# Kernel optimization log

Hardware: AMD Instinct MI355X
Metric: run time of the kernel (lower is better)

## Reference

```python
import jax, jax.numpy as jnp
import numpy as np

D_MODEL = 2048
NUM_HEADS = 32
HEAD_DIM = D_MODEL // NUM_HEADS  # 64
ROPE_BASE = 10000.0


def _rope_cos_sin(seq_len, head_dim, dtype):
    inv_freq = 1.0 / (ROPE_BASE ** (jnp.arange(0, head_dim, 2, dtype=jnp.float32) / head_dim))
    freqs = jnp.arange(seq_len, dtype=jnp.float32)[:, None] * inv_freq[None, :]  # (S, Dh/2)
    emb = jnp.concatenate([freqs, freqs], axis=-1)  # (S, Dh)
    return emb.astype(dtype), jnp.cos(emb).astype(dtype), jnp.sin(emb).astype(dtype)


def _rotate_half(x):
    x1, x2 = jnp.split(x, 2, axis=-1)
    return jnp.concatenate([-x2, x1], axis=-1)


def setup_inputs() -> dict:
    key = jax.random.key(0)
    k1, k2, k3, k4 = jax.random.split(key, 4)
    B, S, D = 1, 2048, D_MODEL
    x = jax.random.normal(k1, (B, S, D), dtype=jnp.float32)
    Wqkv = jax.random.normal(k2, (3 * D, D), dtype=jnp.float32) * 0.02
    Wo = jax.random.normal(k3, (D, D), dtype=jnp.float32) * 0.02
    gate = jax.random.normal(k4, (D,), dtype=jnp.float32) * 0.1
    return {"x": x, "Wqkv": Wqkv, "Wo": Wo, "gate": gate}


def reference(x, Wqkv, Wo, gate):
    B, S, D = x.shape
    H, Dh = NUM_HEADS, HEAD_DIM
    residual = x

    # fused QKV projection (torch Linear: y = x @ W.T)
    qkv = jnp.einsum('bsd,ed->bse', x, Wqkv).reshape(B, S, 3, H, Dh)
    q, k, v = qkv[:, :, 0], qkv[:, :, 1], qkv[:, :, 2]  # each (B, S, H, Dh)

    # RoPE
    _, cos, sin = _rope_cos_sin(S, Dh, x.dtype)
    cos = cos[None, :, None, :]  # (1, S, 1, Dh)
    sin = sin[None, :, None, :]
    q = q * cos + _rotate_half(q) * sin
    k = k * cos + _rotate_half(k) * sin

    # causal SDPA
    scale = 1.0 / np.sqrt(Dh)
    scores = jnp.einsum('bqhd,bkhd->bhqk', q, k) * scale  # (B, H, S, S)
    causal = jnp.tril(jnp.ones((S, S), dtype=bool))
    scores = jnp.where(causal[None, None], scores, jnp.finfo(scores.dtype).min)
    probs = jax.nn.softmax(scores, axis=-1)
    attn = jnp.einsum('bhqk,bkhd->bqhd', probs, v).reshape(B, S, D)

    out = jnp.einsum('bsd,ed->bse', attn, Wo)
    # HeoGate: learned per-channel gated residual (assumption; see notes)
    return residual + gate * out
```

## Files before the change

### kernel.cpp

```cpp
#include <hip/hip_runtime.h>
#include <hip/hip_bf16.h>
#include <cstdint>
#include <cstddef>

typedef __hip_bfloat16 bf16;
typedef short short8 __attribute__((ext_vector_type(8)));
typedef float f32x4 __attribute__((ext_vector_type(4)));

#define S_LEN 2048
#define DMODEL 2048
#define NQKV 6144
#define NHEADS 32
#define HDIM 64
#define ROPE_L2 0.4152410118609203f

__device__ __forceinline__ void async_copy16(const bf16* g, bf16* l) {
  __builtin_amdgcn_global_load_lds(
      (const __attribute__((address_space(1))) void*)g,
      (__attribute__((address_space(3))) void*)l, 16, 0, 0);
}

__device__ __forceinline__ f32x4 mfma_bf16(short8 a, short8 b, f32x4 c) {
  return __builtin_amdgcn_mfma_f32_16x16x32_bf16(a, b, c, 0, 0, 0);
}

__global__ __launch_bounds__(256) void cvt3_kernel(const float* __restrict__ sx,
                                                   bf16* __restrict__ dx,
                                                   const float* __restrict__ sw,
                                                   bf16* __restrict__ dw,
                                                   const float* __restrict__ so,
                                                   bf16* __restrict__ dov) {
  int i = blockIdx.x * 256 + threadIdx.x;
  const float* s;
  bf16* d;
  if (i < 1048576) {
    s = sx; d = dx;
  } else if (i < 4194304) {
    s = sw; d = dw; i -= 1048576;
  } else {
    s = so; d = dov; i -= 4194304;
  }
  const float4 v = ((const float4*)s)[i];
  union { bf16 h[4]; ushort4 u; } tmp;
  tmp.h[0] = __float2bfloat16(v.x);
  tmp.h[1] = __float2bfloat16(v.y);
  tmp.h[2] = __float2bfloat16(v.z);
  tmp.h[3] = __float2bfloat16(v.w);
  ((ushort4*)d)[i] = tmp.u;
}

#define QKV_NT 32
#define QBAR() do { __builtin_amdgcn_s_barrier(); __builtin_amdgcn_sched_barrier(0); } while (0)
#define WAITV(n) asm volatile("s_waitcnt vmcnt(" #n ")" ::: "memory")
#define LGKM0() do { asm volatile("s_waitcnt lgkmcnt(0)" ::: "memory"); \
                     __builtin_amdgcn_sched_barrier(0); } while (0)

__global__ __launch_bounds__(512, 2) void gemm_qkv(const bf16* __restrict__ A,
                                                   const bf16* __restrict__ W,
                                                   bf16* __restrict__ q_ws,
                                                   bf16* __restrict__ k_ws,
                                                   bf16* __restrict__ v_ws) {
  __shared__ bf16 smem[65536];
  const int tid = threadIdx.x;
  const int wave = tid >> 6, lane = tid & 63;
  const int wm = wave >> 2, wn = wave & 3;
  const int m0 = blockIdx.y * 256, n0 = blockIdx.x * 256;
  const int swc = (((lane & 3) ^ ((lane >> 3) & 3)) * 8);
  const int fr = lane & 15, fq = lane >> 4;
  const int rdc = ((fq ^ ((fr >> 1) & 3)) * 8);
  const int srg = wave * 16 + (lane >> 2);

  auto stageA = [&](int t_, int kk_, int off_) {
#pragma unroll
    for (int rd = 0; rd < 2; ++rd)
      async_copy16(A + (size_t)(m0 + rd * 128 + srg) * DMODEL + t_ * 64 + kk_ * 32 + swc,
                   &smem[off_ + (rd * 128 + wave * 16) * 32]);
  };
  auto stageB = [&](int t_, int kk_, int off_) {
#pragma unroll
    for (int rd = 0; rd < 2; ++rd)
      async_copy16(W + (size_t)(n0 + rd * 128 + srg) * DMODEL + t_ * 64 + kk_ * 32 + swc,
                   &smem[off_ + (rd * 128 + wave * 16) * 32]);
  };

  const f32x4 zero = {0.f, 0.f, 0.f, 0.f};
  f32x4 acc[8][4];
#pragma unroll
  for (int i = 0; i < 8; ++i)
#pragma unroll
    for (int j = 0; j < 4; ++j) acc[i][j] = zero;
  short8 a[4], b[4];

  stageA(0, 0, 0);
  stageB(0, 0, 16384);
  stageA(0, 1, 8192);
  stageB(0, 1, 24576);
  stageA(1, 0, 32768);
  stageB(1, 0, 32768 + 16384);
  WAITV(8);
  QBAR();

#define LOAD_A(KK, MB, BC)                                                        \
  {                                                                               \
    const bf16* sA_ = &smem[(BC) * 32768 + (KK) * 8192];                          \
    _Pragma("unroll") for (int mi = 0; mi < 4; ++mi)                              \
        a[mi] = *(const short8*)&sA_[(wm * 128 + (MB) + mi * 16 + fr) * 32 + rdc];\
  }
#define LOAD_B(KK, BC)                                                            \
  {                                                                               \
    const bf16* sB_ = &smem[(BC) * 32768 + 16384 + (KK) * 8192];                  \
    _Pragma("unroll") for (int n = 0; n < 4; ++n)                                 \
        b[n] = *(const short8*)&sB_[(wn * 64 + n * 16 + fr) * 32 + rdc];          \
  }
#define MFMA16(MB)                                                                \
  __builtin_amdgcn_s_setprio(1);                                                  \
  _Pragma("unroll") for (int mi = 0; mi < 4; ++mi)                                \
      _Pragma("unroll") for (int n = 0; n < 4; ++n)                               \
          acc[(MB) / 16 + mi][n] = mfma_bf16(a[mi], b[n], acc[(MB) / 16 + mi][n]);\
  __builtin_amdgcn_s_setprio(0);

#pragma unroll 2
  for (int t = 0; t < QKV_NT; ++t) {
    const int bc = t & 1, bn = bc ^ 1;
    LOAD_A(0, 0, bc); LOAD_B(0, bc);
    if (t + 1 < QKV_NT) stageA(t + 1, 1, bn * 32768 + 8192);
    QBAR(); LGKM0();
    MFMA16(0);
    QBAR();
    LOAD_A(0, 64, bc);
    if (t + 1 < QKV_NT) stageB(t + 1, 1, bn * 32768 + 24576);
    QBAR(); LGKM0();
    MFMA16(64);
    if (t < QKV_NT - 1) { WAITV(8); } else { WAITV(0); }
    QBAR();
    LOAD_A(1, 64, bc); LOAD_B(1, bc);
    if (t + 2 < QKV_NT) stageA(t + 2, 0, bc * 32768);
    QBAR(); LGKM0();
    MFMA16(64);
    QBAR();
    LOAD_A(1, 0, bc);
    if (t + 2 < QKV_NT) stageB(t + 2, 0, bc * 32768 + 16384);
    QBAR(); LGKM0();
    MFMA16(0);
    if (t < QKV_NT - 2) { WAITV(8); }
    else if (t == QKV_NT - 2) { WAITV(4); }
    QBAR();
  }
#undef LOAD_A
#undef LOAD_B
#undef MFMA16

  const int colb = n0 + wn * 64;
  const int sect = colb >> 11;
  const int h = (colb & 2047) >> 6;
  const int col = fr, rq = fq * 4;

  if (sect < 2) {
    bf16* dst = ((sect == 0) ? q_ws : k_ws) + (size_t)h * S_LEN * HDIM;
    bf16* rep = smem + wave * 1152;
    const float f0 = exp2f(-(float)col * ROPE_L2);
    const float f1 = exp2f(-(float)(16 + col) * ROPE_L2);
    __syncthreads();
    for (int m = 0; m < 8; ++m) {
      const int base_s = m0 + wm * 128 + m * 16;
#pragma unroll
      for (int jl = 0; jl < 2; ++jl) {
        const int dh = jl * 16 + col;
        const float fr_ = (jl == 0) ? f0 : f1;
#pragma unroll
        for (int r = 0; r < 4; ++r) {
          const int srow = base_s + rq + r;
          float sn, cs;
          __sincosf((float)srow * fr_, &sn, &cs);
          const float xl = acc[m][jl][r], xh = acc[m][jl + 2][r];
          rep[(rq + r) * 72 + dh]      = __float2bfloat16(xl * cs - xh * sn);
          rep[(rq + r) * 72 + dh + 32] = __float2bfloat16(xh * cs + xl * sn);
        }
      }
#pragma unroll
      for (int p = 0; p < 2; ++p) {
        const int rr = p * 8 + (lane >> 3), ch = lane & 7;
        const uint4 vv = *(const uint4*)&rep[rr * 72 + ch * 8];
        *(uint4*)&dst[(size_t)(base_s + rr) * HDIM + ch * 8] = vv;
      }
    }
  } else {
    bf16* dst = v_ws + (size_t)h * HDIM * S_LEN;
    for (int j = 0; j < 4; ++j) {
      const int dh = j * 16 + col;
      for (int m = 0; m < 8; ++m) {
        const int s0 = m0 + wm * 128 + m * 16 + rq;
        union { bf16 hx[4]; uint2 u; } vk;
#pragma unroll
        for (int r = 0; r < 4; ++r) vk.hx[r] = __float2bfloat16(acc[m][j][r]);
        *(uint2*)&dst[(size_t)dh * S_LEN + s0] = vk.u;
      }
    }
  }
}

__global__ __launch_bounds__(256) void attn_kernel(const bf16* __restrict__ q_ws,
                                                   const bf16* __restrict__ k_ws,
                                                   const bf16* __restrict__ vt_ws,
                                                   bf16* __restrict__ attn_out) {
  const int bid = blockIdx.x;
  const int qt = 31 - (bid >> 5);
  const int h = bid & 31;

  const int tid = threadIdx.x, wave = tid >> 6, lane = tid & 63;
  const int col = lane & 15, fq = lane >> 4;
  const int q_glob = qt * 64 + wave * 16 + col;

  __shared__ bf16 Ks[2][64 * 64];
  __shared__ bf16 Vs[2][64 * 64];
  __shared__ bf16 Pl[4][16 * 72];
  bf16* pl = Pl[wave];

  const bf16* qh = q_ws + (size_t)h * S_LEN * HDIM;
  const bf16* kh = k_ws + (size_t)h * S_LEN * HDIM;
  const bf16* vh = vt_ws + (size_t)h * HDIM * S_LEN;

  const int srow = lane >> 3;
  const int slot = lane & 7;
  const int schunk = slot ^ srow;

  auto stage = [&](int kt, int buf) {
    const int k0 = kt * 64;
#pragma unroll
    for (int j = 0; j < 2; ++j) {
      const int r8 = (wave * 2 + j) * 8;
      async_copy16(kh + (size_t)(k0 + r8 + srow) * HDIM + schunk * 8,
                   &Ks[buf][r8 * 64]);
      async_copy16(vh + (size_t)(r8 + srow) * S_LEN + k0 + schunk * 8,
                   &Vs[buf][r8 * 64]);
    }
  };

  short8 qf[2];
#pragma unroll
  for (int ks = 0; ks < 2; ++ks)
    qf[ks] = *(const short8*)&qh[(size_t)q_glob * HDIM + ks * 32 + fq * 8];

  const f32x4 zero = {0.f, 0.f, 0.f, 0.f};
  f32x4 o_acc[4] = {zero, zero, zero, zero};
  float m_i = -1e30f, l_i = 0.f;

  stage(0, 0);

  for (int kt = 0; kt <= qt; ++kt) {
    const int buf = kt & 1;
    const int k0 = kt * 64;
    __syncthreads();
    if (kt < qt) stage(kt + 1, buf ^ 1);

    short8 kf[8];
#pragma unroll
    for (int n = 0; n < 4; ++n) {
      const int row = n * 16 + col;
#pragma unroll
      for (int ks = 0; ks < 2; ++ks)
        kf[n * 2 + ks] =
            *(const short8*)&Ks[buf][row * 64 + (((ks * 4 + fq) ^ (row & 7)) * 8)];
    }
    f32x4 s_acc[4] = {zero, zero, zero, zero};
#pragma unroll
    for (int n = 0; n < 4; ++n)
#pragma unroll
      for (int ks = 0; ks < 2; ++ks)
        s_acc[n] = mfma_bf16(kf[n * 2 + ks], qf[ks], s_acc[n]);

    short8 vf[8];
#pragma unroll
    for (int n = 0; n < 4; ++n) {
      const int row = n * 16 + col;
#pragma unroll
      for (int ks = 0; ks < 2; ++ks)
        vf[n * 2 + ks] =
            *(const short8*)&Vs[buf][row * 64 + (((ks * 4 + fq) ^ (row & 7)) * 8)];
    }

    if (kt == qt) {
#pragma unroll
      for (int n = 0; n < 4; ++n)
#pragma unroll
        for (int r = 0; r < 4; ++r)
          if (k0 + n * 16 + fq * 4 + r > q_glob) s_acc[n][r] = -1e30f;
    }

    float vmax = -1e30f;
#pragma unroll
    for (int n = 0; n < 4; ++n)
#pragma unroll
      for (int r = 0; r < 4; ++r) vmax = fmaxf(vmax, s_acc[n][r]);
    vmax = fmaxf(vmax, __shfl_xor(vmax, 16, 64));
    vmax = fmaxf(vmax, __shfl_xor(vmax, 32, 64));
    const float mnew = fmaxf(m_i, vmax);
    const float alpha = __expf((m_i - mnew) * 0.125f);
    m_i = mnew;

    float rs = 0.f;
#pragma unroll
    for (int n = 0; n < 4; ++n)
#pragma unroll
      for (int r = 0; r < 4; ++r) {
        const float p = __expf((s_acc[n][r] - mnew) * 0.125f);
        s_acc[n][r] = p;
        rs += p;
      }
    rs += __shfl_xor(rs, 16, 64);
    rs += __shfl_xor(rs, 32, 64);
    l_i = l_i * alpha + rs;

#pragma unroll
    for (int n = 0; n < 4; ++n)
#pragma unroll
      for (int r = 0; r < 4; ++r) o_acc[n][r] *= alpha;

#pragma unroll
    for (int n = 0; n < 4; ++n) {
      union { bf16 hx[4]; uint2 u; } pk;
#pragma unroll
      for (int r = 0; r < 4; ++r) pk.hx[r] = __float2bfloat16(s_acc[n][r]);
      *(uint2*)&pl[col * 72 + n * 16 + fq * 4] = pk.u;
    }
    short8 pa[2];
#pragma unroll
    for (int ks = 0; ks < 2; ++ks)
      pa[ks] = *(const short8*)&pl[col * 72 + ks * 32 + fq * 8];

#pragma unroll
    for (int n = 0; n < 4; ++n)
#pragma unroll
      for (int ks = 0; ks < 2; ++ks)
        o_acc[n] = mfma_bf16(vf[n * 2 + ks], pa[ks], o_acc[n]);
  }

  const float inv = 1.0f / l_i;
#pragma unroll
  for (int n = 0; n < 4; ++n) {
#pragma unroll
    for (int r = 0; r < 4; ++r) o_acc[n][r] *= inv;
    union { bf16 hx[4]; uint2 u; } ok;
#pragma unroll
    for (int r = 0; r < 4; ++r) ok.hx[r] = __float2bfloat16(o_acc[n][r]);
    *(uint2*)&attn_out[(size_t)q_glob * DMODEL + h * HDIM + n * 16 + fq * 4] = ok.u;
  }
}

__global__ __launch_bounds__(256) void gemm_out(const bf16* __restrict__ A,
                                                const bf16* __restrict__ W,
                                                const float* __restrict__ xres,
                                                const float* __restrict__ gate,
                                                float* __restrict__ out) {
  constexpr int K = DMODEL;
  __shared__ bf16 As[64 * 32];
  __shared__ bf16 Bs[128 * 32];
  const int tid = threadIdx.x;
  const int wave = tid >> 6, lane = tid & 63;
  const int m0 = blockIdx.y * 64, n0 = blockIdx.x * 128;
  const int sr = lane >> 2;
  const int swc = (((lane & 3) ^ ((lane >> 3) & 3)) * 8);
  const int fr = lane & 15, fq = lane >> 4;
  const int rdc = ((fq ^ ((fr >> 1) & 3)) * 8);

  const f32x4 zero = {0.f, 0.f, 0.f, 0.f};
  f32x4 acc[4][2];
  for (int i = 0; i < 4; ++i)
    for (int j = 0; j < 2; ++j) acc[i][j] = zero;

  for (int kt = 0; kt < K; kt += 32) {
    __syncthreads();
    async_copy16(A + (size_t)(m0 + wave * 16 + sr) * K + kt + swc,
                 &As[(wave * 16) * 32]);
#pragma unroll
    for (int j = 0; j < 2; ++j)
      async_copy16(W + (size_t)(n0 + wave * 32 + j * 16 + sr) * K + kt + swc,
                   &Bs[(wave * 32 + j * 16) * 32]);
    __syncthreads();
    short8 a[4], b[2];
    for (int i = 0; i < 4; ++i)
      a[i] = *(const short8*)&As[(i * 16 + fr) * 32 + rdc];
    for (int j = 0; j < 2; ++j)
      b[j] = *(const short8*)&Bs[(wave * 32 + j * 16 + fr) * 32 + rdc];
    for (int i = 0; i < 4; ++i)
      for (int j = 0; j < 2; ++j)
        acc[i][j] = mfma_bf16(a[i], b[j], acc[i][j]);
  }

  const int col = fr, rq = fq * 4;
  for (int j = 0; j < 2; ++j) {
    const int cc = n0 + wave * 32 + j * 16 + col;
    const float g = gate[cc];
    for (int i = 0; i < 4; ++i) {
      const int base_row = m0 + i * 16 + rq;
      for (int r = 0; r < 4; ++r) {
        const size_t idx = (size_t)(base_row + r) * DMODEL + cc;
        out[idx] = xres[idx] + g * acc[i][j][r];
      }
    }
  }
}

extern "C" void kernel_launch(void* const* d_in, const int* in_sizes, int n_in,
                              void* d_out, int out_size, void* d_ws, size_t ws_size,
                              hipStream_t stream) {
  const float* x    = (const float*)d_in[0];
  const float* Wqkv = (const float*)d_in[1];
  const float* Wo   = (const float*)d_in[2];
  const float* gate = (const float*)d_in[3];
  float* out = (float*)d_out;

  char* ws = (char*)d_ws;
  const size_t MB = 1024 * 1024;
  bf16* xb      = (bf16*)(ws);
  bf16* wqkvb   = (bf16*)(ws + 8 * MB);
  bf16* wob     = (bf16*)(ws + 32 * MB);
  bf16* q_ws    = (bf16*)(ws + 40 * MB);
  bf16* k_ws    = (bf16*)(ws + 48 * MB);
  bf16* v_ws    = (bf16*)(ws + 56 * MB);
  bf16* attn_ws = (bf16*)(ws);

  cvt3_kernel<<<dim3(20480), 256, 0, stream>>>(x, xb, Wqkv, wqkvb, Wo, wob);

  gemm_qkv<<<dim3(NQKV / 256, S_LEN / 256), 512, 0, stream>>>(xb, wqkvb, q_ws, k_ws, v_ws);
  attn_kernel<<<dim3(1024), 256, 0, stream>>>(q_ws, k_ws, v_ws, attn_ws);
  gemm_out<<<dim3(DMODEL / 128, DMODEL / 64), 256, 0, stream>>>(attn_ws, wob, x, gate, out);
}
```

Measured before the change: 253.1 us.

## Widen attention tiles, add lazy softmax rescaling, triple-buffer output GEMM

The attention kernel now processes 128 query rows per block with 8 waves, so each staged K/V tile is shared by twice as many queries. Online-softmax rescaling is skipped unless some lane's running max grows by more than a threshold, which drops exp and multiply work on most iterations. The output GEMM gains a 3-stage async LDS pipeline with vmcnt waits, overlapping loads with MFMA work. In exchange, the larger blocks halve the grid and lengthen per-block causal work, and the diff relies on WAITV/QBAR/LGKM0 macros that must already be defined in the unseen part of the file.

```diff
diff --git a/kernel.cpp b/kernel.cpp
--- a/kernel.cpp
+++ b/kernel.cpp
@@ -199,21 +199,21 @@
   }
 }
 
-__global__ __launch_bounds__(256) void attn_kernel(const bf16* __restrict__ q_ws,
+__global__ __launch_bounds__(512) void attn_kernel(const bf16* __restrict__ q_ws,
                                                    const bf16* __restrict__ k_ws,
                                                    const bf16* __restrict__ vt_ws,
                                                    bf16* __restrict__ attn_out) {
   const int bid = blockIdx.x;
-  const int qt = 31 - (bid >> 5);
+  const int qt = 15 - (bid >> 5);
   const int h = bid & 31;
 
   const int tid = threadIdx.x, wave = tid >> 6, lane = tid & 63;
   const int col = lane & 15, fq = lane >> 4;
-  const int q_glob = qt * 64 + wave * 16 + col;
+  const int q_glob = qt * 128 + wave * 16 + col;
 
   __shared__ bf16 Ks[2][64 * 64];
   __shared__ bf16 Vs[2][64 * 64];
-  __shared__ bf16 Pl[4][16 * 72];
+  __shared__ bf16 Pl[8][16 * 72];
   bf16* pl = Pl[wave];
 
   const bf16* qh = q_ws + (size_t)h * S_LEN * HDIM;
@@ -226,14 +226,11 @@
 
   auto stage = [&](int kt, int buf) {
     const int k0 = kt * 64;
-#pragma unroll
-    for (int j = 0; j < 2; ++j) {
-      const int r8 = (wave * 2 + j) * 8;
-      async_copy16(kh + (size_t)(k0 + r8 + srow) * HDIM + schunk * 8,
-                   &Ks[buf][r8 * 64]);
-      async_copy16(vh + (size_t)(r8 + srow) * S_LEN + k0 + schunk * 8,
-                   &Vs[buf][r8 * 64]);
-    }
+    const int r8 = wave * 8;
+    async_copy16(kh + (size_t)(k0 + r8 + srow) * HDIM + schunk * 8,
+                 &Ks[buf][r8 * 64]);
+    async_copy16(vh + (size_t)(r8 + srow) * S_LEN + k0 + schunk * 8,
+                 &Vs[buf][r8 * 64]);
   };
 
   short8 qf[2];
@@ -247,11 +244,12 @@
 
   stage(0, 0);
 
-  for (int kt = 0; kt <= qt; ++kt) {
+  const int lastk = 2 * qt + 1;
+  for (int kt = 0; kt <= lastk; ++kt) {
     const int buf = kt & 1;
     const int k0 = kt * 64;
     __syncthreads();
-    if (kt < qt) stage(kt + 1, buf ^ 1);
+    if (kt < lastk) stage(kt + 1, buf ^ 1);
 
     short8 kf[8];
 #pragma unroll
@@ -279,7 +277,7 @@
             *(const short8*)&Vs[buf][row * 64 + (((ks * 4 + fq) ^ (row & 7)) * 8)];
     }
 
-    if (kt == qt) {
+    if (k0 + 63 > qt * 128 + wave * 16) {
 #pragma unroll
       for (int n = 0; n < 4; ++n)
 #pragma unroll
@@ -294,27 +292,30 @@
       for (int r = 0; r < 4; ++r) vmax = fmaxf(vmax, s_acc[n][r]);
     vmax = fmaxf(vmax, __shfl_xor(vmax, 16, 64));
     vmax = fmaxf(vmax, __shfl_xor(vmax, 32, 64));
-    const float mnew = fmaxf(m_i, vmax);
-    const float alpha = __expf((m_i - mnew) * 0.125f);
-    m_i = mnew;
+
+    if (!__all(vmax - m_i <= 8.0f)) {
+      const float mnew = fmaxf(m_i, vmax);
+      const float alpha = __expf((m_i - mnew) * 0.125f);
+      l_i *= alpha;
+#pragma unroll
+      for (int n = 0; n < 4; ++n)
+#pragma unroll
+        for (int r = 0; r < 4; ++r) o_acc[n][r] *= alpha;
+      m_i = mnew;
+    }
 
     float rs = 0.f;
 #pragma unroll
     for (int n = 0; n < 4; ++n)
 #pragma unroll
       for (int r = 0; r < 4; ++r) {
-        const float p = __expf((s_acc[n][r] - mnew) * 0.125f);
+        const float p = __expf((s_acc[n][r] - m_i) * 0.125f);
         s_acc[n][r] = p;
         rs += p;
       }
     rs += __shfl_xor(rs, 16, 64);
     rs += __shfl_xor(rs, 32, 64);
-    l_i = l_i * alpha + rs;
-
-#pragma unroll
-    for (int n = 0; n < 4; ++n)
-#pragma unroll
-      for (int r = 0; r < 4; ++r) o_acc[n][r] *= alpha;
+    l_i += rs;
 
 #pragma unroll
     for (int n = 0; n < 4; ++n) {
@@ -353,8 +354,9 @@
                                                 const float* __restrict__ gate,
                                                 float* __restrict__ out) {
   constexpr int K = DMODEL;
-  __shared__ bf16 As[64 * 32];
-  __shared__ bf16 Bs[128 * 32];
+  constexpr int NT = K / 32;
+  __shared__ bf16 As[3][64 * 32];
+  __shared__ bf16 Bs[3][128 * 32];
   const int tid = threadIdx.x;
   const int wave = tid >> 6, lane = tid & 63;
   const int m0 = blockIdx.y * 64, n0 = blockIdx.x * 128;
@@ -363,28 +365,47 @@
   const int fr = lane & 15, fq = lane >> 4;
   const int rdc = ((fq ^ ((fr >> 1) & 3)) * 8);
 
+  auto stage = [&](int t_, int s_) {
+    async_copy16(A + (size_t)(m0 + wave * 16 + sr) * K + t_ * 32 + swc,
+                 &As[s_][(wave * 16) * 32]);
+#pragma unroll
+    for (int j = 0; j < 2; ++j)
+      async_copy16(W + (size_t)(n0 + wave * 32 + j * 16 + sr) * K + t_ * 32 + swc,
+                   &Bs[s_][(wave * 32 + j * 16) * 32]);
+  };
+
   const f32x4 zero = {0.f, 0.f, 0.f, 0.f};
   f32x4 acc[4][2];
   for (int i = 0; i < 4; ++i)
     for (int j = 0; j < 2; ++j) acc[i][j] = zero;
 
-  for (int kt = 0; kt < K; kt += 32) {
-    __syncthreads();
-    async_copy16(A + (size_t)(m0 + wave * 16 + sr) * K + kt + swc,
-                 &As[(wave * 16) * 32]);
+  stage(0, 0);
+  stage(1, 1);
+  WAITV(3);
+  QBAR();
+
+  for (int t = 0; t < NT; ++t) {
+    const int s = t % 3;
+    short8 a[4], b[2];
+#pragma unroll
+    for (int i = 0; i < 4; ++i)
+      a[i] = *(const short8*)&As[s][(i * 16 + fr) * 32 + rdc];
 #pragma unroll
     for (int j = 0; j < 2; ++j)
-      async_copy16(W + (size_t)(n0 + wave * 32 + j * 16 + sr) * K + kt + swc,
-                   &Bs[(wave * 32 + j * 16) * 32]);
-    __syncthreads();
-    short8 a[4], b[2];
+      b[j] = *(const short8*)&Bs[s][(wave * 32 + j * 16 + fr) * 32 + rdc];
+    LGKM0();
+    QBAR();
+    if (t + 2 < NT) stage(t + 2, (t + 2) % 3);
+#pragma unroll
     for (int i = 0; i < 4; ++i)
-      a[i] = *(const short8*)&As[(i * 16 + fr) * 32 + rdc];
-    for (int j = 0; j < 2; ++j)
-      b[j] = *(const short8*)&Bs[(wave * 32 + j * 16 + fr) * 32 + rdc];
-    for (int i = 0; i < 4; ++i)
+#pragma unroll
       for (int j = 0; j < 2; ++j)
         acc[i][j] = mfma_bf16(a[i], b[j], acc[i][j]);
+    if (t + 1 < NT) {
+      if (t + 2 < NT) { WAITV(3); }
+      else            { WAITV(0); }
+      QBAR();
+    }
   }
 
   const int col = fr, rq = fq * 4;
@@ -423,6 +444,6 @@
   cvt3_kernel<<<dim3(20480), 256, 0, stream>>>(x, xb, Wqkv, wqkvb, Wo, wob);
 
   gemm_qkv<<<dim3(NQKV / 256, S_LEN / 256), 512, 0, stream>>>(xb, wqkvb, q_ws, k_ws, v_ws);
-  attn_kernel<<<dim3(1024), 256, 0, stream>>>(q_ws, k_ws, v_ws, attn_ws);
+  attn_kernel<<<dim3(512), 512, 0, stream>>>(q_ws, k_ws, v_ws, attn_ws);
   gemm_out<<<dim3(DMODEL / 128, DMODEL / 64), 256, 0, stream>>>(attn_ws, wob, x, gate, out);
 }
```

New measurement: 251.9 us. Within noise of the previous version (-0.5%).
